# Optimization experiments

Hardware: AMD Instinct MI355X
Metric: run time of the kernel (lower is better)

Reference implementation:

```python
import jax, jax.numpy as jnp
import numpy as np

B, S, H, NH, DH, I, C, P = 4, 1024, 1280, 20, 64, 5120, 13, 8
LN_EPS = 1e-5


def setup_inputs() -> dict:
    key = jax.random.key(0)
    ks = jax.random.split(key, 20)
    n = lambda k, shp, s=0.02: (jax.random.normal(k, shp, jnp.float32) * s)
    return {
        "hidden_states": jax.random.normal(ks[0], (B, S, H), jnp.float32),
        "attention_mask": jnp.ones((B, S), jnp.float32),
        "Wq": n(ks[1], (H, H)), "bq": jnp.zeros((H,), jnp.float32),
        "Wk": n(ks[2], (H, H)), "bk": jnp.zeros((H,), jnp.float32),
        "Wv": n(ks[3], (H, H)), "bv": jnp.zeros((H,), jnp.float32),
        "W_ct1": n(ks[4], (P, C), 0.3), "b_ct1": jnp.zeros((P,), jnp.float32),
        "W_ct2": n(ks[5], (P, C), 0.3), "b_ct2": jnp.zeros((P,), jnp.float32),
        "M": n(ks[6], (C, C), 0.5),
        "bias_scale": jnp.full((1,), 0.5, jnp.float32),
        "W_ptm": n(ks[7], (P, H)), "b_ptm": jnp.zeros((P,), jnp.float32),
        "ln_g": jnp.ones((H,), jnp.float32), "ln_b": jnp.zeros((H,), jnp.float32),
        "Wf1": n(ks[8], (I, H)), "bf1": jnp.zeros((I,), jnp.float32),
        "Wf2": n(ks[9], (H, I)), "bf2": jnp.zeros((H,), jnp.float32),
    }


def reference(hidden_states, attention_mask, Wq, bq, Wk, bk, Wv, bv,
              W_ct1, b_ct1, W_ct2, b_ct2, M, bias_scale, W_ptm, b_ptm,
              ln_g, ln_b, Wf1, bf1, Wf2, bf2):
    h = hidden_states
    # crosstalk bilinear projection: (P,C) @ (C,P) -> (P,P)
    out1 = (M.T @ W_ct1.T + b_ct1).T          # (P, C)
    out2 = M @ W_ct2.T + b_ct2                # (C, P)
    R = out1 @ out2                           # (P, P)
    # ptm_predictor (Linear H->P) + softmax
    ptm = jax.nn.softmax(h @ W_ptm.T + b_ptm, axis=-1)            # (B,S,P)
    Bb = jnp.tanh(jnp.einsum('blc,cd,bmd->blm', ptm, R, ptm)) * bias_scale  # (B,S,S)
    # manual multi-head attention
    q = (h @ Wq.T + bq).reshape(B, S, NH, DH).transpose(0, 2, 1, 3)
    k = (h @ Wk.T + bk).reshape(B, S, NH, DH).transpose(0, 2, 1, 3)
    v = (h @ Wv.T + bv).reshape(B, S, NH, DH).transpose(0, 2, 1, 3)
    scores = jnp.einsum('bhld,bhmd->bhlm', q, k) / np.float32(np.sqrt(DH))
    scores = scores + Bb[:, None]
    scores = scores + (1.0 - attention_mask)[:, None, None, :] * jnp.finfo(h.dtype).min
    probs = jax.nn.softmax(scores, axis=-1)
    ctx = jnp.einsum('bhlm,bhmd->bhld', probs, v)
    ctx = ctx.transpose(0, 2, 1, 3).reshape(B, S, H)
    # residual + LayerNorm
    x = h + ctx
    mu = jnp.mean(x, -1, keepdims=True)
    var = jnp.var(x, -1, keepdims=True)
    x = (x - mu) * jax.lax.rsqrt(var + LN_EPS) * ln_g + ln_b
    # FFN with exact GELU, residual
    ff = jax.nn.gelu(x @ Wf1.T + bf1, approximate=False) @ Wf2.T + bf2
    return x + ff
```

## Files before the change

### kernel.cpp

```cpp
#include <hip/hip_runtime.h>
#include <math.h>

typedef _Float16 f16;
typedef _Float16 f16x2 __attribute__((ext_vector_type(2)));
typedef _Float16 f16x8 __attribute__((ext_vector_type(8)));
typedef _Float16 f16x4 __attribute__((ext_vector_type(4)));
typedef float f32x4 __attribute__((ext_vector_type(4)));

#define B_ 4
#define S_ 1024
#define H_ 1280
#define NH_ 20
#define DH_ 64
#define I_ 5120
#define C_ 13
#define P_ 8
#define LOG2E 1.44269504088896f

__device__ __forceinline__ void store_val(float* p, float v) { *p = v; }
__device__ __forceinline__ void store_val(f16* p, float v) { *p = (f16)v; }

__global__ __launch_bounds__(256) void cvt6_kernel(
    const float* __restrict__ s0, f16* __restrict__ d0, int n0,
    const float* __restrict__ s1, f16* __restrict__ d1, int n1,
    const float* __restrict__ s2, f16* __restrict__ d2, int n2,
    const float* __restrict__ s3, f16* __restrict__ d3, int n3,
    const float* __restrict__ s4, f16* __restrict__ d4, int n4,
    const float* __restrict__ s5, f16* __restrict__ d5, int n5) {
    int seg = blockIdx.y;
    const float* src = (seg == 0) ? s0 : (seg == 1) ? s1 : (seg == 2) ? s2
                     : (seg == 3) ? s3 : (seg == 4) ? s4 : s5;
    f16* dst = (seg == 0) ? d0 : (seg == 1) ? d1 : (seg == 2) ? d2
             : (seg == 3) ? d3 : (seg == 4) ? d4 : d5;
    int n = (seg == 0) ? n0 : (seg == 1) ? n1 : (seg == 2) ? n2
          : (seg == 3) ? n3 : (seg == 4) ? n4 : n5;
    int i = blockIdx.x * 256 + threadIdx.x;
    if (i < n) {
        f32x4 v = ((const f32x4*)src)[i];
        f16x4 o;
#pragma unroll
        for (int e = 0; e < 4; e++) o[e] = (f16)v[e];
        ((f16x4*)dst)[i] = o;
    }
}

__global__ __launch_bounds__(256) void ptm_kernel(const float* __restrict__ hin,
                                                  const float* __restrict__ Wptm,
                                                  const float* __restrict__ bptm,
                                                  const float* __restrict__ Mg,
                                                  const float* __restrict__ W1,
                                                  const float* __restrict__ b1,
                                                  const float* __restrict__ W2,
                                                  const float* __restrict__ b2,
                                                  float* __restrict__ ptm,
                                                  float* __restrict__ tg) {
    __shared__ float o1[P_][C_];
    __shared__ float o2[C_][P_];
    __shared__ float R[P_ * P_];
    int t = threadIdx.x;
    if (t < P_ * C_) {
        int p = t / C_, c = t % C_;
        float s = b1[p];
        for (int k = 0; k < C_; k++) s += Mg[k * C_ + c] * W1[p * C_ + k];
        o1[p][c] = s;
        int c2 = t / P_, p2 = t % P_;
        float s2 = b2[p2];
        for (int k = 0; k < C_; k++) s2 += Mg[c2 * C_ + k] * W2[p2 * C_ + k];
        o2[c2][p2] = s2;
    }
    __syncthreads();
    if (t < P_ * P_) {
        int p = t >> 3, q = t & 7;
        float s = 0.f;
        for (int c = 0; c < C_; c++) s += o1[p][c] * o2[c][q];
        R[t] = s;
    }
    __syncthreads();

    int wv = t >> 6, lane = t & 63;
    int row = blockIdx.x * 4 + wv;
    const float* hrow = hin + (size_t)row * H_;
    float acc[P_] = {};
    for (int i = 0; i < H_ / 64; i++) {
        int k = lane + 64 * i;
        float hv = hrow[k];
#pragma unroll
        for (int p = 0; p < P_; p++) acc[p] += hv * Wptm[p * H_ + k];
    }
#pragma unroll
    for (int p = 0; p < P_; p++) {
#pragma unroll
        for (int o = 32; o >= 1; o >>= 1) acc[p] += __shfl_xor(acc[p], o);
        acc[p] += bptm[p];
    }
    float mx = acc[0];
#pragma unroll
    for (int p = 1; p < P_; p++) mx = fmaxf(mx, acc[p]);
    float sum = 0.f;
#pragma unroll
    for (int p = 0; p < P_; p++) { acc[p] = expf(acc[p] - mx); sum += acc[p]; }
    float rinv = 1.f / sum;
#pragma unroll
    for (int p = 0; p < P_; p++) acc[p] *= rinv;
    float tv[P_];
#pragma unroll
    for (int d = 0; d < P_; d++) {
        float s = 0.f;
#pragma unroll
        for (int c = 0; c < P_; c++) s += acc[c] * R[c * P_ + d];
        tv[d] = s;
    }
    if (lane == 0) {
#pragma unroll
        for (int p = 0; p < P_; p++) {
            ptm[(size_t)row * P_ + p] = acc[p];
            tg[(size_t)row * P_ + p]  = tv[p];
        }
    }
}

__global__ __launch_bounds__(256) void bias_kernel(const float* __restrict__ tg,
                                                   const float* __restrict__ ptm,
                                                   const float* __restrict__ mask,
                                                   const float* __restrict__ bscale_p,
                                                   f16* __restrict__ bb) {
    const int bl = blockIdx.x;
    const int b = bl >> 10;
    const int t = threadIdx.x;
    __shared__ float tl[P_];
    if (t < P_) tl[t] = tg[(size_t)bl * P_ + t];
    __syncthreads();
    const float bscale = bscale_p[0];
    float t0 = tl[0], t1 = tl[1], t2 = tl[2], t3 = tl[3];
    float t4 = tl[4], t5 = tl[5], t6 = tl[6], t7 = tl[7];
#pragma unroll
    for (int i = 0; i < 4; i++) {
        int m = t + 256 * i;
        const float* pm = ptm + ((size_t)b * S_ + m) * P_;
        float4 p0 = *(const float4*)pm;
        float4 p1 = *(const float4*)(pm + 4);
        float d = t0 * p0.x + t1 * p0.y + t2 * p0.z + t3 * p0.w
                + t4 * p1.x + t5 * p1.y + t6 * p1.z + t7 * p1.w;
        float v = (tanhf(d) * bscale + (1.0f - mask[(size_t)b * S_ + m]) * (-30000.0f)) * LOG2E;
        bb[(size_t)bl * S_ + m] = (f16)v;
    }
}

template <int MODE, typename YT>
__device__ __forceinline__ void gemm_body(const f16* __restrict__ X,
                                          const f16* __restrict__ W,
                                          const float* __restrict__ bias,
                                          YT* __restrict__ Y,
                                          const f16* __restrict__ res,
                                          int Ndim, int Kdim, int kbeg, int kend,
                                          int m0, int n0, f16* sA, f16* sB) {
    const int t = threadIdx.x;
    const int lane = t & 63, w = t >> 6;
    const int wr = w >> 1, wc = w & 1;
    const int lr = lane & 15, kq = lane >> 4;

    f32x4 acc[4][4] = {};

    int s_row[4], s_gc[4];
#pragma unroll
    for (int inst = 0; inst < 4; inst++) {
        int ci = t + 256 * inst;
        s_row[inst] = ci >> 3;
        s_gc[inst] = (ci & 7) ^ (s_row[inst] & 7);
    }

    for (int k0 = kbeg; k0 < kend; k0 += 64) {
        __syncthreads();
#pragma unroll
        for (int inst = 0; inst < 4; inst++) {
            int ci = t + 256 * inst;
            __builtin_amdgcn_global_load_lds(
                (const unsigned*)(X + (size_t)(m0 + s_row[inst]) * Kdim + k0 + s_gc[inst] * 8),
                (unsigned*)(sA + ci * 8), 16, 0, 0);
        }
#pragma unroll
        for (int inst = 0; inst < 4; inst++) {
            int ci = t + 256 * inst;
            __builtin_amdgcn_global_load_lds(
                (const unsigned*)(W + (size_t)(n0 + s_row[inst]) * Kdim + k0 + s_gc[inst] * 8),
                (unsigned*)(sB + ci * 8), 16, 0, 0);
        }
        __syncthreads();
#pragma unroll
        for (int ks = 0; ks < 2; ks++) {
            f16x8 af[4], bf[4];
#pragma unroll
            for (int i = 0; i < 4; i++) {
                int row = wr * 64 + i * 16 + lr;
                int cl = (ks * 4 + kq) ^ (row & 7);
                af[i] = *(const f16x8*)(sA + row * 64 + cl * 8);
            }
#pragma unroll
            for (int j = 0; j < 4; j++) {
                int row = wc * 64 + j * 16 + lr;
                int cl = (ks * 4 + kq) ^ (row & 7);
                bf[j] = *(const f16x8*)(sB + row * 64 + cl * 8);
            }
#pragma unroll
            for (int i = 0; i < 4; i++)
#pragma unroll
                for (int j = 0; j < 4; j++)
                    acc[i][j] = __builtin_amdgcn_mfma_f32_16x16x32_f16(af[i], bf[j], acc[i][j], 0, 0, 0);
        }
    }
#pragma unroll
    for (int j = 0; j < 4; j++) {
        int col = n0 + wc * 64 + j * 16 + lr;
        float bcol = (MODE == 3) ? 0.f : bias[col];
#pragma unroll
        for (int i = 0; i < 4; i++) {
#pragma unroll
            for (int rr = 0; rr < 4; rr++) {
                int row = m0 + wr * 64 + i * 16 + kq * 4 + rr;
                float v = acc[i][j][rr] + bcol;
                if (MODE == 1) v = 0.5f * v * (1.0f + erff(v * 0.70710678118654752f));
                if (MODE == 2) v += (float)res[(size_t)row * Ndim + col];
                store_val(&Y[(size_t)row * Ndim + col], v);
            }
        }
    }
}

template <int MODE, typename YT>
__global__ __launch_bounds__(256, 2) void gemm128(const f16* __restrict__ X,
                                                  const f16* __restrict__ W,
                                                  const float* __restrict__ bias,
                                                  YT* __restrict__ Y,
                                                  const f16* __restrict__ res,
                                                  int Ndim, int Kdim) {
    __shared__ f16 sA[128 * 64];
    __shared__ f16 sB[128 * 64];
    gemm_body<MODE, YT>(X, W, bias, Y, res, Ndim, Kdim, 0, Kdim,
                        blockIdx.x * 128, blockIdx.y * 128, sA, sB);
}

__global__ __launch_bounds__(256, 2) void gemm_sk(const f16* __restrict__ X,
                                                  const f16* __restrict__ W,
                                                  float* __restrict__ Pb,
                                                  int Ndim, int Kdim, int Mdim) {
    __shared__ f16 sA[128 * 64];
    __shared__ f16 sB[128 * 64];
    const int kd2 = Kdim >> 1;
    float* Y = Pb + (size_t)blockIdx.z * Mdim * Ndim;
    gemm_body<3, float>(X, W, nullptr, Y, nullptr, Ndim, Kdim,
                        blockIdx.z * kd2, blockIdx.z * kd2 + kd2,
                        blockIdx.x * 128, blockIdx.y * 128, sA, sB);
}

__global__ __launch_bounds__(256) void reduce2_kernel(const float* __restrict__ p0,
                                                      const float* __restrict__ p1,
                                                      const float* __restrict__ bias,
                                                      const f16* __restrict__ res,
                                                      float* __restrict__ out) {
    int i = blockIdx.x * 256 + threadIdx.x;
    int col = (i * 4) % H_;
    f32x4 a = ((const f32x4*)p0)[i];
    f32x4 b = ((const f32x4*)p1)[i];
    f32x4 bc = *(const f32x4*)(bias + col);
    f16x4 r = ((const f16x4*)res)[i];
    f32x4 o;
#pragma unroll
    for (int e = 0; e < 4; e++) o[e] = a[e] + b[e] + bc[e] + (float)r[e];
    ((f32x4*)out)[i] = o;
}

__global__ __launch_bounds__(256, 2) void gemm_qkv(const f16* __restrict__ X,
                                                   const f16* __restrict__ Wq,
                                                   const f16* __restrict__ Wk,
                                                   const f16* __restrict__ Wv,
                                                   const float* __restrict__ bq,
                                                   const float* __restrict__ bk,
                                                   const float* __restrict__ bv,
                                                   f16* __restrict__ qb,
                                                   f16* __restrict__ kb,
                                                   f16* __restrict__ vb) {
    __shared__ f16 sA[128 * 64];
    __shared__ f16 sB[128 * 64];
    const int g = blockIdx.y / 10, nt = blockIdx.y % 10;
    const f16* W = (g == 0) ? Wq : (g == 1) ? Wk : Wv;
    const float* bias = (g == 0) ? bq : (g == 1) ? bk : bv;
    f16* Y = (g == 0) ? qb : (g == 1) ? kb : vb;
    gemm_body<0, f16>(X, W, bias, Y, nullptr, H_, H_, 0, H_,
                      blockIdx.x * 128, nt * 128, sA, sB);
}

__global__ __launch_bounds__(256) void attn_kernel(const f16* __restrict__ q,
                                                   const f16* __restrict__ k,
                                                   const f16* __restrict__ v,
                                                   const f16* __restrict__ bb,
                                                   const float* __restrict__ hin,
                                                   float* __restrict__ xpre) {
    __shared__ f16 sQ[64 * 72];
    __shared__ f16 sK[64 * 72];
    __shared__ f16 sVT[64 * 72];
    __shared__ f16 sP[64 * 72];

    const int t = threadIdx.x;
    const int w = t >> 6, lane = t & 63;
    const int lr = lane & 15, kq = lane >> 4;
    const int l0 = blockIdx.x * 64;
    const int h = blockIdx.y, b = blockIdx.z;
    const size_t base = (size_t)b * S_ * H_ + (size_t)h * DH_;

    for (int idx = t; idx < 512; idx += 256) {
        int r = idx >> 3, c8 = (idx & 7) * 8;
        f16x8 qv = *(const f16x8*)&q[base + (size_t)(l0 + r) * H_ + c8];
#pragma unroll
        for (int e = 0; e < 8; e++) qv[e] = (f16)((float)qv[e] * (0.125f * LOG2E));
        *(f16x8*)&sQ[r * 72 + c8] = qv;
    }
    __syncthreads();
    f16x8 afq[2];
    afq[0] = *(const f16x8*)&sQ[(w * 16 + lr) * 72 + kq * 8];
    afq[1] = *(const f16x8*)&sQ[(w * 16 + lr) * 72 + 32 + kq * 8];

    f32x4 acc_o[4] = {};
    float lstate[4] = {};

    const int vr2 = (t >> 3) * 2, vc8 = (t & 7) * 8;
    const int vmsw = vr2 ^ vc8;

    for (int mt = 0; mt < 16; mt++) {
        const int m0 = mt * 64;
        __syncthreads();
        for (int idx = t; idx < 512; idx += 256) {
            int r = idx >> 3, c8 = (idx & 7) * 8;
            f16x8 kvv = *(const f16x8*)&k[base + (size_t)(m0 + r) * H_ + c8];
            *(f16x8*)&sK[r * 72 + c8] = kvv;
        }
        {
            f16x8 v0 = *(const f16x8*)&v[base + (size_t)(m0 + vr2) * H_ + vc8];
            f16x8 v1 = *(const f16x8*)&v[base + (size_t)(m0 + vr2 + 1) * H_ + vc8];
#pragma unroll
            for (int e = 0; e < 8; e++) {
                f16x2 pk = {v0[e], v1[e]};
                *(f16x2*)&sVT[(vc8 + e) * 72 + vmsw] = pk;
            }
        }
        __syncthreads();

        f32x4 sacc[4] = {};
#pragma unroll
        for (int ks = 0; ks < 2; ks++)
#pragma unroll
            for (int j = 0; j < 4; j++) {
                f16x8 bk = *(const f16x8*)&sK[(j * 16 + lr) * 72 + ks * 32 + kq * 8];
                sacc[j] = __builtin_amdgcn_mfma_f32_16x16x32_f16(afq[ks], bk, sacc[j], 0, 0, 0);
            }
        const f16* bbrow = bb + ((size_t)b * S_ + l0 + w * 16 + kq * 4) * S_ + m0;
#pragma unroll
        for (int j = 0; j < 4; j++)
#pragma unroll
            for (int rr = 0; rr < 4; rr++)
                sacc[j][rr] += (float)bbrow[(size_t)rr * S_ + j * 16 + lr];

#pragma unroll
        for (int j = 0; j < 4; j++)
#pragma unroll
            for (int rr = 0; rr < 4; rr++) {
                float p = __builtin_exp2f(sacc[j][rr]);
                lstate[rr] += p;
                sP[(w * 16 + kq * 4 + rr) * 72 + j * 16 + lr] = (f16)p;
            }
        __syncthreads();

        f16x8 ap[2];
        ap[0] = *(const f16x8*)&sP[(w * 16 + lr) * 72 + kq * 8];
        ap[1] = *(const f16x8*)&sP[(w * 16 + lr) * 72 + 32 + kq * 8];
#pragma unroll
        for (int ks = 0; ks < 2; ks++)
#pragma unroll
            for (int j2 = 0; j2 < 4; j2++) {
                int d = j2 * 16 + lr;
                int s_ = (d >> 3) & 7;
                f16x8 bv = *(const f16x8*)&sVT[d * 72 + 8 * (((ks << 2) + kq) ^ s_)];
                acc_o[j2] = __builtin_amdgcn_mfma_f32_16x16x32_f16(ap[ks], bv, acc_o[j2], 0, 0, 0);
            }
    }

#pragma unroll
    for (int rr = 0; rr < 4; rr++) {
#pragma unroll
        for (int off = 8; off >= 1; off >>= 1) lstate[rr] += __shfl_xor(lstate[rr], off);
    }

#pragma unroll
    for (int rr = 0; rr < 4; rr++) {
        float linv = 1.0f / lstate[rr];
        int tok = l0 + w * 16 + kq * 4 + rr;
        size_t obase = base + (size_t)tok * H_;
#pragma unroll
        for (int j2 = 0; j2 < 4; j2++) {
            int d = j2 * 16 + lr;
            xpre[obase + d] = hin[obase + d] + acc_o[j2][rr] * linv;
        }
    }
}

__global__ __launch_bounds__(256) void ln_kernel(const float* __restrict__ xpre,
                                                 const float* __restrict__ g,
                                                 const float* __restrict__ bb,
                                                 f16* __restrict__ xln) {
    int row = blockIdx.x, t = threadIdx.x;
    const float* xr = xpre + (size_t)row * H_;
    float xv[5], s1 = 0.f, s2 = 0.f;
#pragma unroll
    for (int i = 0; i < 5; i++) {
        float v = xr[t + 256 * i];
        xv[i] = v; s1 += v; s2 += v * v;
    }
#pragma unroll
    for (int o = 32; o >= 1; o >>= 1) { s1 += __shfl_xor(s1, o); s2 += __shfl_xor(s2, o); }
    __shared__ float r1[4], r2[4];
    int wv = t >> 6, lane = t & 63;
    if (lane == 0) { r1[wv] = s1; r2[wv] = s2; }
    __syncthreads();
    float m1 = (r1[0] + r1[1] + r1[2] + r1[3]) * (1.0f / H_);
    float m2 = (r2[0] + r2[1] + r2[2] + r2[3]) * (1.0f / H_);
    float rstd = rsqrtf(m2 - m1 * m1 + 1e-5f);
#pragma unroll
    for (int i = 0; i < 5; i++) {
        int c = t + 256 * i;
        float v = (xv[i] - m1) * rstd * g[c] + bb[c];
        xln[(size_t)row * H_ + c] = (f16)v;
    }
}

extern "C" void kernel_launch(void* const* d_in, const int* in_sizes, int n_in,
                              void* d_out, int out_size, void* d_ws, size_t ws_size,
                              hipStream_t stream) {
    (void)in_sizes; (void)n_in; (void)out_size; (void)ws_size;
    const float* hin  = (const float*)d_in[0];
    const float* mask = (const float*)d_in[1];
    const float* Wq = (const float*)d_in[2];  const float* bq = (const float*)d_in[3];
    const float* Wk = (const float*)d_in[4];  const float* bk = (const float*)d_in[5];
    const float* Wv = (const float*)d_in[6];  const float* bv = (const float*)d_in[7];
    const float* Wct1 = (const float*)d_in[8];  const float* bct1 = (const float*)d_in[9];
    const float* Wct2 = (const float*)d_in[10]; const float* bct2 = (const float*)d_in[11];
    const float* Mg = (const float*)d_in[12];   const float* bscale = (const float*)d_in[13];
    const float* Wptm = (const float*)d_in[14]; const float* bptm = (const float*)d_in[15];
    const float* lng = (const float*)d_in[16];  const float* lnb = (const float*)d_in[17];
    const float* Wf1 = (const float*)d_in[18];  const float* bf1 = (const float*)d_in[19];
    const float* Wf2 = (const float*)d_in[20];  const float* bf2 = (const float*)d_in[21];

    char* ws = (char*)d_ws;
    const size_t SZ_PT  = (size_t)B_ * S_ * P_ * 4;
    const size_t SZ_H16 = (size_t)B_ * S_ * H_ * 2;
    const size_t SZ_H32 = (size_t)B_ * S_ * H_ * 4;
    const size_t SZ_WH  = (size_t)H_ * H_ * 2;
    const size_t SZ_WI  = (size_t)I_ * H_ * 2;
    float* ptm  = (float*)(ws + 256);
    float* tg   = (float*)(ws + 256 + SZ_PT);
    char* A0    = ws + 256 + 2 * SZ_PT;
    f16* hin16  = (f16*)(A0);
    f16* qb     = (f16*)(A0 + SZ_H16);
    f16* kb     = (f16*)(A0 + 2 * SZ_H16);
    f16* vb     = (f16*)(A0 + 3 * SZ_H16);
    float* xpre = (float*)(A0 + 4 * SZ_H16);
    f16* xln    = (f16*)(A0 + 4 * SZ_H16 + SZ_H32);
    f16* bbias  = (f16*)(A0 + 5 * SZ_H16 + SZ_H32);
    char* WA    = A0 + 5 * SZ_H16 + SZ_H32 + (size_t)B_ * S_ * S_ * 2;
    f16* Wq16   = (f16*)(WA);
    f16* Wk16   = (f16*)(WA + SZ_WH);
    f16* Wv16   = (f16*)(WA + 2 * SZ_WH);
    f16* Wf116  = (f16*)(WA + 3 * SZ_WH);
    f16* Wf216  = (f16*)(WA + 3 * SZ_WH + SZ_WI);
    f16* g1     = (f16*)(A0);
    float* pbuf = (float*)(WA + 3 * SZ_WH + 2 * SZ_WI);

    const int NH4 = (B_ * S_ * H_) / 4, NW4 = (H_ * H_) / 4, NI4 = (I_ * H_) / 4;
    cvt6_kernel<<<dim3((NI4 + 255) / 256, 6), 256, 0, stream>>>(
        hin, hin16, NH4, Wq, Wq16, NW4, Wk, Wk16, NW4,
        Wv, Wv16, NW4, Wf1, Wf116, NI4, Wf2, Wf216, NI4);

    ptm_kernel<<<S_ * B_ / 4, 256, 0, stream>>>(hin, Wptm, bptm,
                                                Mg, Wct1, bct1, Wct2, bct2, ptm, tg);
    bias_kernel<<<B_ * S_, 256, 0, stream>>>(tg, ptm, mask, bscale, bbias);
    gemm_qkv<<<dim3(32, 30), 256, 0, stream>>>(hin16, Wq16, Wk16, Wv16, bq, bk, bv, qb, kb, vb);
    attn_kernel<<<dim3(S_ / 64, NH_, B_), 256, 0, stream>>>(qb, kb, vb, bbias, hin, xpre);
    ln_kernel<<<B_ * S_, 256, 0, stream>>>(xpre, lng, lnb, xln);
    gemm128<1, f16><<<dim3(32, I_ / 128), 256, 0, stream>>>(xln, Wf116, bf1, g1, nullptr, I_, H_);
    gemm_sk<<<dim3(32, 10, 2), 256, 0, stream>>>(g1, Wf216, pbuf, H_, I_, B_ * S_);
    reduce2_kernel<<<(B_ * S_ * H_) / 4 / 256, 256, 0, stream>>>(
        pbuf, pbuf + (size_t)B_ * S_ * H_, bf2, xln, (float*)d_out);
}
```

Measured before the change: 468.0 us.

## Replace 128x128 GEMMs with double-buffered 256x256 tile, 512-thread pipelined kernel

Replaces the single-buffered 128x128 GEMM body with a 256x256 tile computed by 8 waves. It double-buffers LDS and splits each K step into four phases, interleaving async global->LDS loads with MFMA bursts under raised s_setprio. The FFN2 split-K goes from 2-way to 3-way, reusing the xpre buffer as the third partial, so the reduce kernel sums three partials. The aim is more data reuse per loaded byte and overlap of memory with compute. In exchange the grids get smaller (e.g. 240 blocks for QKV, 240 for FFN2) and wave quantization on 256 CUs could worsen.

```diff
diff --git a/kernel.cpp b/kernel.cpp
--- a/kernel.cpp
+++ b/kernel.cpp
@@ -147,79 +147,165 @@
 }
 
 template <int MODE, typename YT>
-__device__ __forceinline__ void gemm_body(const f16* __restrict__ X,
-                                          const f16* __restrict__ W,
-                                          const float* __restrict__ bias,
-                                          YT* __restrict__ Y,
-                                          const f16* __restrict__ res,
-                                          int Ndim, int Kdim, int kbeg, int kend,
-                                          int m0, int n0, f16* sA, f16* sB) {
+__device__ __forceinline__ void gemm256_body(const f16* __restrict__ X,
+                                             const f16* __restrict__ W,
+                                             const float* __restrict__ bias,
+                                             YT* __restrict__ Y,
+                                             const f16* __restrict__ res,
+                                             int Ndim, int Kdim, int kbeg, int kend,
+                                             int m0, int n0, f16* sA, f16* sB) {
     const int t = threadIdx.x;
-    const int lane = t & 63, w = t >> 6;
-    const int wr = w >> 1, wc = w & 1;
+    const int lane = t & 63;
+    const int w = t >> 6;
+    const int wr = w >> 2, wc = w & 3;
     const int lr = lane & 15, kq = lane >> 4;
-
-    f32x4 acc[4][4] = {};
-
-    int s_row[4], s_gc[4];
-#pragma unroll
-    for (int inst = 0; inst < 4; inst++) {
-        int ci = t + 256 * inst;
-        s_row[inst] = ci >> 3;
-        s_gc[inst] = (ci & 7) ^ (s_row[inst] & 7);
-    }
-
-    for (int k0 = kbeg; k0 < kend; k0 += 64) {
-        __syncthreads();
-#pragma unroll
-        for (int inst = 0; inst < 4; inst++) {
-            int ci = t + 256 * inst;
-            __builtin_amdgcn_global_load_lds(
-                (const unsigned*)(X + (size_t)(m0 + s_row[inst]) * Kdim + k0 + s_gc[inst] * 8),
-                (unsigned*)(sA + ci * 8), 16, 0, 0);
-        }
-#pragma unroll
-        for (int inst = 0; inst < 4; inst++) {
-            int ci = t + 256 * inst;
-            __builtin_amdgcn_global_load_lds(
-                (const unsigned*)(W + (size_t)(n0 + s_row[inst]) * Kdim + k0 + s_gc[inst] * 8),
-                (unsigned*)(sB + ci * 8), 16, 0, 0);
-        }
-        __syncthreads();
-#pragma unroll
-        for (int ks = 0; ks < 2; ks++) {
-            f16x8 af[4], bf[4];
-#pragma unroll
-            for (int i = 0; i < 4; i++) {
-                int row = wr * 64 + i * 16 + lr;
-                int cl = (ks * 4 + kq) ^ (row & 7);
-                af[i] = *(const f16x8*)(sA + row * 64 + cl * 8);
-            }
-#pragma unroll
-            for (int j = 0; j < 4; j++) {
-                int row = wc * 64 + j * 16 + lr;
-                int cl = (ks * 4 + kq) ^ (row & 7);
-                bf[j] = *(const f16x8*)(sB + row * 64 + cl * 8);
-            }
-#pragma unroll
-            for (int i = 0; i < 4; i++)
-#pragma unroll
-                for (int j = 0; j < 4; j++)
-                    acc[i][j] = __builtin_amdgcn_mfma_f32_16x16x32_f16(af[i], bf[j], acc[i][j], 0, 0, 0);
-        }
-    }
-#pragma unroll
-    for (int j = 0; j < 4; j++) {
-        int col = n0 + wc * 64 + j * 16 + lr;
-        float bcol = (MODE == 3) ? 0.f : bias[col];
-#pragma unroll
-        for (int i = 0; i < 4; i++) {
-#pragma unroll
-            for (int rr = 0; rr < 4; rr++) {
-                int row = m0 + wr * 64 + i * 16 + kq * 4 + rr;
+    const int NT = (kend - kbeg) >> 6;
+
+    const int rh0 = t >> 3;
+    const int gc0 = (t & 7) ^ (rh0 & 7);
+    const f16* Asrc = X + (size_t)(m0 + rh0) * Kdim + kbeg + gc0 * 8;
+    const f16* Bsrc = W + (size_t)(n0 + rh0) * Kdim + kbeg + gc0 * 8;
+
+    f32x4 acc[8][4] = {};
+
+#define STAGE_A(bufsel, h, kt_) do {                                           \
+        const f16* s_ = Asrc + (size_t)(h) * 128 * Kdim + (kt_) * 64;          \
+        f16* d_ = sA + (bufsel) * 16384 + (h) * 8192 + t * 8;                  \
+        __builtin_amdgcn_global_load_lds((const unsigned*)s_, (unsigned*)d_, 16, 0, 0); \
+        __builtin_amdgcn_global_load_lds((const unsigned*)(s_ + (size_t)64 * Kdim), \
+                                         (unsigned*)(d_ + 4096), 16, 0, 0);    \
+    } while (0)
+#define STAGE_B(bufsel, h, kt_) do {                                           \
+        const f16* s_ = Bsrc + (size_t)(h) * 128 * Kdim + (kt_) * 64;          \
+        f16* d_ = sB + (bufsel) * 16384 + (h) * 8192 + t * 8;                  \
+        __builtin_amdgcn_global_load_lds((const unsigned*)s_, (unsigned*)d_, 16, 0, 0); \
+        __builtin_amdgcn_global_load_lds((const unsigned*)(s_ + (size_t)64 * Kdim), \
+                                         (unsigned*)(d_ + 4096), 16, 0, 0);    \
+    } while (0)
+
+    STAGE_A(0, 0, 0); STAGE_A(0, 1, 0);
+    STAGE_B(0, 0, 0); STAGE_B(0, 1, 0);
+    if (NT > 1) {
+        STAGE_A(1, 0, 1); STAGE_A(1, 1, 1);
+        asm volatile("s_waitcnt vmcnt(4)");
+    } else {
+        asm volatile("s_waitcnt vmcnt(0)");
+    }
+    __builtin_amdgcn_s_barrier();
+
+    for (int kt = 0; kt < NT; ++kt) {
+        const int p = kt & 1;
+        const f16* cA = sA + p * 16384;
+        const f16* cB = sB + p * 16384;
+        f16x8 a[4][2], b0[2][2], b1[2][2];
+
+#pragma unroll
+        for (int i = 0; i < 4; ++i) {
+            const int r = wr * 128 + (i + 4) * 16 + lr;
+#pragma unroll
+            for (int ks = 0; ks < 2; ++ks) {
+                const int cl = (ks * 4 + kq) ^ (r & 7);
+                a[i][ks] = *(const f16x8*)(cA + r * 64 + cl * 8);
+            }
+        }
+#pragma unroll
+        for (int j = 0; j < 2; ++j) {
+            const int rb = wc * 64 + j * 16 + lr;
+#pragma unroll
+            for (int ks = 0; ks < 2; ++ks) {
+                const int cl = (ks * 4 + kq) ^ (rb & 7);
+                b0[j][ks] = *(const f16x8*)(cB + rb * 64 + cl * 8);
+            }
+        }
+        if (kt + 1 < NT) STAGE_B(p ^ 1, 0, kt + 1);
+        __builtin_amdgcn_s_barrier();
+        __builtin_amdgcn_s_setprio(1);
+#pragma unroll
+        for (int ks = 0; ks < 2; ++ks)
+#pragma unroll
+            for (int i = 0; i < 4; ++i)
+#pragma unroll
+                for (int j = 0; j < 2; ++j)
+                    acc[i + 4][j] = __builtin_amdgcn_mfma_f32_16x16x32_f16(
+                        a[i][ks], b0[j][ks], acc[i + 4][j], 0, 0, 0);
+        __builtin_amdgcn_s_setprio(0);
+        __builtin_amdgcn_s_barrier();
+
+#pragma unroll
+        for (int j = 0; j < 2; ++j) {
+            const int rb = wc * 64 + (j + 2) * 16 + lr;
+#pragma unroll
+            for (int ks = 0; ks < 2; ++ks) {
+                const int cl = (ks * 4 + kq) ^ (rb & 7);
+                b1[j][ks] = *(const f16x8*)(cB + rb * 64 + cl * 8);
+            }
+        }
+        if (kt + 1 < NT) STAGE_B(p ^ 1, 1, kt + 1);
+        __builtin_amdgcn_s_barrier();
+        __builtin_amdgcn_s_setprio(1);
+#pragma unroll
+        for (int ks = 0; ks < 2; ++ks)
+#pragma unroll
+            for (int i = 0; i < 4; ++i)
+#pragma unroll
+                for (int j = 0; j < 2; ++j)
+                    acc[i + 4][j + 2] = __builtin_amdgcn_mfma_f32_16x16x32_f16(
+                        a[i][ks], b1[j][ks], acc[i + 4][j + 2], 0, 0, 0);
+        __builtin_amdgcn_s_setprio(0);
+        __builtin_amdgcn_s_barrier();
+
+#pragma unroll
+        for (int i = 0; i < 4; ++i) {
+            const int r = wr * 128 + i * 16 + lr;
+#pragma unroll
+            for (int ks = 0; ks < 2; ++ks) {
+                const int cl = (ks * 4 + kq) ^ (r & 7);
+                a[i][ks] = *(const f16x8*)(cA + r * 64 + cl * 8);
+            }
+        }
+        __builtin_amdgcn_s_barrier();
+        if (kt + 2 < NT) STAGE_A(p, 0, kt + 2);
+        __builtin_amdgcn_s_setprio(1);
+#pragma unroll
+        for (int ks = 0; ks < 2; ++ks)
+#pragma unroll
+            for (int i = 0; i < 4; ++i)
+#pragma unroll
+                for (int j = 0; j < 2; ++j)
+                    acc[i][j] = __builtin_amdgcn_mfma_f32_16x16x32_f16(
+                        a[i][ks], b0[j][ks], acc[i][j], 0, 0, 0);
+        __builtin_amdgcn_s_setprio(0);
+        __builtin_amdgcn_s_barrier();
+
+        if (kt + 2 < NT) STAGE_A(p, 1, kt + 2);
+        __builtin_amdgcn_s_setprio(1);
+#pragma unroll
+        for (int ks = 0; ks < 2; ++ks)
+#pragma unroll
+            for (int i = 0; i < 4; ++i)
+#pragma unroll
+                for (int j = 0; j < 2; ++j)
+                    acc[i][j + 2] = __builtin_amdgcn_mfma_f32_16x16x32_f16(
+                        a[i][ks], b1[j][ks], acc[i][j + 2], 0, 0, 0);
+        __builtin_amdgcn_s_setprio(0);
+        if (kt + 2 < NT) asm volatile("s_waitcnt vmcnt(4)");
+        else             asm volatile("s_waitcnt vmcnt(0)");
+        __builtin_amdgcn_s_barrier();
+    }
+#undef STAGE_A
+#undef STAGE_B
+
+#pragma unroll
+    for (int j = 0; j < 4; ++j) {
+        const int col = n0 + wc * 64 + j * 16 + lr;
+        const float bcol = (MODE == 3) ? 0.f : bias[col];
+#pragma unroll
+        for (int i = 0; i < 8; ++i) {
+#pragma unroll
+            for (int rr = 0; rr < 4; ++rr) {
+                const int row = m0 + wr * 128 + i * 16 + kq * 4 + rr;
                 float v = acc[i][j][rr] + bcol;
                 if (MODE == 1) v = 0.5f * v * (1.0f + erff(v * 0.70710678118654752f));
-                if (MODE == 2) v += (float)res[(size_t)row * Ndim + col];
                 store_val(&Y[(size_t)row * Ndim + col], v);
             }
         }
@@ -227,33 +313,57 @@
 }
 
 template <int MODE, typename YT>
-__global__ __launch_bounds__(256, 2) void gemm128(const f16* __restrict__ X,
+__global__ __launch_bounds__(512, 2) void gemm256(const f16* __restrict__ X,
                                                   const f16* __restrict__ W,
                                                   const float* __restrict__ bias,
                                                   YT* __restrict__ Y,
-                                                  const f16* __restrict__ res,
                                                   int Ndim, int Kdim) {
-    __shared__ f16 sA[128 * 64];
-    __shared__ f16 sB[128 * 64];
-    gemm_body<MODE, YT>(X, W, bias, Y, res, Ndim, Kdim, 0, Kdim,
-                        blockIdx.x * 128, blockIdx.y * 128, sA, sB);
-}
-
-__global__ __launch_bounds__(256, 2) void gemm_sk(const f16* __restrict__ X,
-                                                  const f16* __restrict__ W,
-                                                  float* __restrict__ Pb,
-                                                  int Ndim, int Kdim, int Mdim) {
-    __shared__ f16 sA[128 * 64];
-    __shared__ f16 sB[128 * 64];
-    const int kd2 = Kdim >> 1;
-    float* Y = Pb + (size_t)blockIdx.z * Mdim * Ndim;
-    gemm_body<3, float>(X, W, nullptr, Y, nullptr, Ndim, Kdim,
-                        blockIdx.z * kd2, blockIdx.z * kd2 + kd2,
-                        blockIdx.x * 128, blockIdx.y * 128, sA, sB);
-}
-
-__global__ __launch_bounds__(256) void reduce2_kernel(const float* __restrict__ p0,
+    __shared__ f16 sA[2 * 16384];
+    __shared__ f16 sB[2 * 16384];
+    gemm256_body<MODE, YT>(X, W, bias, Y, nullptr, Ndim, Kdim, 0, Kdim,
+                           blockIdx.x * 256, blockIdx.y * 256, sA, sB);
+}
+
+__global__ __launch_bounds__(512, 2) void gemm256_qkv(const f16* __restrict__ X,
+                                                      const f16* __restrict__ Wq,
+                                                      const f16* __restrict__ Wk,
+                                                      const f16* __restrict__ Wv,
+                                                      const float* __restrict__ bq,
+                                                      const float* __restrict__ bk,
+                                                      const float* __restrict__ bv,
+                                                      f16* __restrict__ qb,
+                                                      f16* __restrict__ kb,
+                                                      f16* __restrict__ vb) {
+    __shared__ f16 sA[2 * 16384];
+    __shared__ f16 sB[2 * 16384];
+    const int nt = blockIdx.y;
+    const int g = nt / 5, c = nt % 5;
+    const f16* W = (g == 0) ? Wq : (g == 1) ? Wk : Wv;
+    const float* bias = (g == 0) ? bq : (g == 1) ? bk : bv;
+    f16* Y = (g == 0) ? qb : (g == 1) ? kb : vb;
+    gemm256_body<0, f16>(X, W, bias, Y, nullptr, H_, H_, 0, H_,
+                         blockIdx.x * 256, c * 256, sA, sB);
+}
+
+__global__ __launch_bounds__(512, 2) void gemm256_sk(const f16* __restrict__ X,
+                                                     const f16* __restrict__ W,
+                                                     float* __restrict__ p0,
+                                                     float* __restrict__ p1,
+                                                     float* __restrict__ p2,
+                                                     int Ndim, int Kdim) {
+    __shared__ f16 sA[2 * 16384];
+    __shared__ f16 sB[2 * 16384];
+    const int z = blockIdx.z;
+    float* Y = (z == 0) ? p0 : (z == 1) ? p1 : p2;
+    const int kbeg = z * 1728;
+    const int kend = (z == 2) ? Kdim : kbeg + 1728;
+    gemm256_body<3, float>(X, W, nullptr, Y, nullptr, Ndim, Kdim, kbeg, kend,
+                           blockIdx.x * 256, blockIdx.y * 256, sA, sB);
+}
+
+__global__ __launch_bounds__(256) void reduce3_kernel(const float* __restrict__ p0,
                                                       const float* __restrict__ p1,
+                                                      const float* __restrict__ p2,
                                                       const float* __restrict__ bias,
                                                       const f16* __restrict__ res,
                                                       float* __restrict__ out) {
@@ -261,32 +371,13 @@
     int col = (i * 4) % H_;
     f32x4 a = ((const f32x4*)p0)[i];
     f32x4 b = ((const f32x4*)p1)[i];
+    f32x4 c = ((const f32x4*)p2)[i];
     f32x4 bc = *(const f32x4*)(bias + col);
     f16x4 r = ((const f16x4*)res)[i];
     f32x4 o;
 #pragma unroll
-    for (int e = 0; e < 4; e++) o[e] = a[e] + b[e] + bc[e] + (float)r[e];
+    for (int e = 0; e < 4; e++) o[e] = a[e] + b[e] + c[e] + bc[e] + (float)r[e];
     ((f32x4*)out)[i] = o;
-}
-
-__global__ __launch_bounds__(256, 2) void gemm_qkv(const f16* __restrict__ X,
-                                                   const f16* __restrict__ Wq,
-                                                   const f16* __restrict__ Wk,
-                                                   const f16* __restrict__ Wv,
-                                                   const float* __restrict__ bq,
-                                                   const float* __restrict__ bk,
-                                                   const float* __restrict__ bv,
-                                                   f16* __restrict__ qb,
-                                                   f16* __restrict__ kb,
-                                                   f16* __restrict__ vb) {
-    __shared__ f16 sA[128 * 64];
-    __shared__ f16 sB[128 * 64];
-    const int g = blockIdx.y / 10, nt = blockIdx.y % 10;
-    const f16* W = (g == 0) ? Wq : (g == 1) ? Wk : Wv;
-    const float* bias = (g == 0) ? bq : (g == 1) ? bk : bv;
-    f16* Y = (g == 0) ? qb : (g == 1) ? kb : vb;
-    gemm_body<0, f16>(X, W, bias, Y, nullptr, H_, H_, 0, H_,
-                      blockIdx.x * 128, nt * 128, sA, sB);
 }
 
 __global__ __launch_bounds__(256) void attn_kernel(const f16* __restrict__ q,
@@ -481,11 +572,13 @@
     ptm_kernel<<<S_ * B_ / 4, 256, 0, stream>>>(hin, Wptm, bptm,
                                                 Mg, Wct1, bct1, Wct2, bct2, ptm, tg);
     bias_kernel<<<B_ * S_, 256, 0, stream>>>(tg, ptm, mask, bscale, bbias);
-    gemm_qkv<<<dim3(32, 30), 256, 0, stream>>>(hin16, Wq16, Wk16, Wv16, bq, bk, bv, qb, kb, vb);
+    gemm256_qkv<<<dim3(16, 15), 512, 0, stream>>>(hin16, Wq16, Wk16, Wv16,
+                                                  bq, bk, bv, qb, kb, vb);
     attn_kernel<<<dim3(S_ / 64, NH_, B_), 256, 0, stream>>>(qb, kb, vb, bbias, hin, xpre);
     ln_kernel<<<B_ * S_, 256, 0, stream>>>(xpre, lng, lnb, xln);
-    gemm128<1, f16><<<dim3(32, I_ / 128), 256, 0, stream>>>(xln, Wf116, bf1, g1, nullptr, I_, H_);
-    gemm_sk<<<dim3(32, 10, 2), 256, 0, stream>>>(g1, Wf216, pbuf, H_, I_, B_ * S_);
-    reduce2_kernel<<<(B_ * S_ * H_) / 4 / 256, 256, 0, stream>>>(
-        pbuf, pbuf + (size_t)B_ * S_ * H_, bf2, xln, (float*)d_out);
-}
+    gemm256<1, f16><<<dim3(16, I_ / 256), 512, 0, stream>>>(xln, Wf116, bf1, g1, I_, H_);
+    gemm256_sk<<<dim3(16, H_ / 256, 3), 512, 0, stream>>>(
+        g1, Wf216, pbuf, pbuf + (size_t)B_ * S_ * H_, xpre, H_, I_);
+    reduce3_kernel<<<(B_ * S_ * H_) / 4 / 256, 256, 0, stream>>>(
+        pbuf, pbuf + (size_t)B_ * S_ * H_, xpre, bf2, xln, (float*)d_out);
+}
```

New measurement: 510.1 us. 1.09x slower.

## Prefetch next K/V tile into registers and remap attention blocks across XCDs

Applied to the files above, without the earlier changes.

The attention kernel now loads the next K and V tiles from global memory into registers while the current tile is being computed, then writes them to shared memory at the top of the next iteration. This hides global load latency behind the MFMA work. It also remaps the block index so consecutive work items for the same head and batch land on the same XCD, which should improve L2 reuse of K/V. In exchange it uses more registers, and the last iteration issues a redundant wrap-around load.

```diff
diff --git a/kernel.cpp b/kernel.cpp
--- a/kernel.cpp
+++ b/kernel.cpp
@@ -303,9 +303,21 @@
     const int t = threadIdx.x;
     const int w = t >> 6, lane = t & 63;
     const int lr = lane & 15, kq = lane >> 4;
-    const int l0 = blockIdx.x * 64;
-    const int h = blockIdx.y, b = blockIdx.z;
+    const int gid = blockIdx.x + 16 * (blockIdx.y + 20 * blockIdx.z);
+    const int wk = (gid & 7) * 160 + (gid >> 3);
+    const int l0 = (wk & 15) * 64;
+    const int hb = wk >> 4;
+    const int h = hb % 20, b = hb / 20;
     const size_t base = (size_t)b * S_ * H_ + (size_t)h * DH_;
+
+    const int kr0 = t >> 3, kc8 = (t & 7) * 8;
+    const int vr2 = (t >> 3) * 2, vc8 = (t & 7) * 8;
+    const int vmsw = vr2 ^ vc8;
+
+    f16x8 kA0 = *(const f16x8*)&k[base + (size_t)kr0 * H_ + kc8];
+    f16x8 kA1 = *(const f16x8*)&k[base + (size_t)(kr0 + 32) * H_ + kc8];
+    f16x8 vA0 = *(const f16x8*)&v[base + (size_t)vr2 * H_ + vc8];
+    f16x8 vA1 = *(const f16x8*)&v[base + (size_t)(vr2 + 1) * H_ + vc8];
 
     for (int idx = t; idx < 512; idx += 256) {
         int r = idx >> 3, c8 = (idx & 7) * 8;
@@ -322,26 +334,21 @@
     f32x4 acc_o[4] = {};
     float lstate[4] = {};
 
-    const int vr2 = (t >> 3) * 2, vc8 = (t & 7) * 8;
-    const int vmsw = vr2 ^ vc8;
-
     for (int mt = 0; mt < 16; mt++) {
         const int m0 = mt * 64;
         __syncthreads();
-        for (int idx = t; idx < 512; idx += 256) {
-            int r = idx >> 3, c8 = (idx & 7) * 8;
-            f16x8 kvv = *(const f16x8*)&k[base + (size_t)(m0 + r) * H_ + c8];
-            *(f16x8*)&sK[r * 72 + c8] = kvv;
-        }
-        {
-            f16x8 v0 = *(const f16x8*)&v[base + (size_t)(m0 + vr2) * H_ + vc8];
-            f16x8 v1 = *(const f16x8*)&v[base + (size_t)(m0 + vr2 + 1) * H_ + vc8];
-#pragma unroll
-            for (int e = 0; e < 8; e++) {
-                f16x2 pk = {v0[e], v1[e]};
-                *(f16x2*)&sVT[(vc8 + e) * 72 + vmsw] = pk;
-            }
-        }
+        *(f16x8*)&sK[kr0 * 72 + kc8] = kA0;
+        *(f16x8*)&sK[(kr0 + 32) * 72 + kc8] = kA1;
+#pragma unroll
+        for (int e = 0; e < 8; e++) {
+            f16x2 pk = {vA0[e], vA1[e]};
+            *(f16x2*)&sVT[(vc8 + e) * 72 + vmsw] = pk;
+        }
+        const int m1 = ((mt + 1) & 15) * 64;
+        f16x8 kB0 = *(const f16x8*)&k[base + (size_t)(m1 + kr0) * H_ + kc8];
+        f16x8 kB1 = *(const f16x8*)&k[base + (size_t)(m1 + kr0 + 32) * H_ + kc8];
+        f16x8 vB0 = *(const f16x8*)&v[base + (size_t)(m1 + vr2) * H_ + vc8];
+        f16x8 vB1 = *(const f16x8*)&v[base + (size_t)(m1 + vr2 + 1) * H_ + vc8];
         __syncthreads();
 
         f32x4 sacc[4] = {};
@@ -381,6 +388,7 @@
                 f16x8 bv = *(const f16x8*)&sVT[d * 72 + 8 * (((ks << 2) + kq) ^ s_)];
                 acc_o[j2] = __builtin_amdgcn_mfma_f32_16x16x32_f16(ap[ks], bv, acc_o[j2], 0, 0, 0);
             }
+        kA0 = kB0; kA1 = kB1; vA0 = vB0; vA1 = vB1;
     }
 
 #pragma unroll
```

Measured after the change: 482.7 us. 3.1% more time.
